# Performance work log

Measured on AMD Instinct MI355X. Metric: run time of the kernel, lower is better.

The kernel has to match this reference:

```python
import jax, jax.numpy as jnp
import numpy as np

D_MODEL = 2048
N_HEADS = 16
HEAD_DIM = D_MODEL // N_HEADS
SEGMENT_SIZE = 512
DILATION = 2
BATCH = 2
SEQ_LEN = 8192


def setup_inputs() -> dict:
    key = jax.random.key(0)
    k1, k2, k3 = jax.random.split(key, 3)
    x = jax.random.normal(k1, (BATCH, SEQ_LEN, D_MODEL), dtype=jnp.float32)
    Wqkv = jax.random.normal(k2, (3 * D_MODEL, D_MODEL), dtype=jnp.float32) * 0.02
    b_qkv = jnp.zeros((3 * D_MODEL,), dtype=jnp.float32)
    Wout = jax.random.normal(k3, (D_MODEL, D_MODEL), dtype=jnp.float32) * 0.02
    b_out = jnp.zeros((D_MODEL,), dtype=jnp.float32)
    return {"x": x, "Wqkv": Wqkv, "b_qkv": b_qkv, "Wout": Wout, "b_out": b_out}


def reference(x, Wqkv, b_qkv, Wout, b_out):
    B, S, D = x.shape
    H, hd = N_HEADS, HEAD_DIM
    # dilated segment gather: [B, n_seg, seg, D] strided by dilation -> [B, n_seg, L, D]
    xs = x.reshape(B, -1, SEGMENT_SIZE, D)[:, :, ::DILATION, :]
    N, L = xs.shape[1], xs.shape[2]
    # fused qkv projection (FlashMHA.Wqkv)
    qkv = jnp.einsum('bnld,ed->bnle', xs, Wqkv) + b_qkv  # [B,N,L,3D]
    q, k, v = jnp.split(qkv, 3, axis=-1)
    q = q.reshape(B, N, L, H, hd)
    k = k.reshape(B, N, L, H, hd)
    v = v.reshape(B, N, L, H, hd)
    scale = 1.0 / jnp.sqrt(jnp.asarray(hd, dtype=x.dtype))
    # per-segment attention over the dilated tokens
    scores = jnp.einsum('bnqhd,bnkhd->bnhqk', q, k) * scale  # [B,N,H,L,L]
    attn = jax.nn.softmax(scores, axis=-1)
    out = jnp.einsum('bnhqk,bnkhd->bnqhd', attn, v).reshape(B, N, L, D)
    # output projection (FlashMHA.out_proj)
    out = jnp.einsum('bnld,ed->bnle', out, Wout) + b_out
    # merge segments back: [B, N*L, D]
    return out.reshape(B, -1, D)
```

## Files before the change

kernel.cpp:

```cpp
#include <hip/hip_runtime.h>
#include <hip/hip_bf16.h>
#include <stdint.h>

#define DEVI __device__ __forceinline__

typedef __attribute__((ext_vector_type(8))) short bf16x8;
typedef __attribute__((ext_vector_type(4))) float f32x4;


DEVI unsigned short f2bf(float f) {
  unsigned int u = __float_as_uint(f);
  return (unsigned short)((u + 0x7fffu + ((u >> 16) & 1u)) >> 16);
}

DEVI void load_lds16(const void* g, void* l) {
  __builtin_amdgcn_global_load_lds(
      (const __attribute__((address_space(1))) unsigned int*)g,
      (__attribute__((address_space(3))) unsigned int*)l, 16, 0, 0);
}

DEVI bf16x8 ld8(const unsigned short* p) {
  return *reinterpret_cast<const bf16x8*>(p);
}

__global__ void k_prep(const float* __restrict__ x, unsigned short* __restrict__ xs,
                       const float* __restrict__ Wqkv, unsigned short* __restrict__ wq,
                       const float* __restrict__ Wout, unsigned short* __restrict__ wo) {
  const int bid = blockIdx.x;
  const float* src;
  unsigned short* dst;
  long i;
  if (bid < 16384) {
    int ii = bid * 256 + threadIdx.x;
    int r = ii >> 9;
    int c = (ii & 511) << 2;
    int b = r >> 12;
    int rem = r & 4095;
    int seg = rem >> 8;
    int lcl = rem & 255;
    long src_row = (long)b * 8192 + seg * 512 + lcl * 2;
    const float4 v = *reinterpret_cast<const float4*>(x + src_row * 2048 + c);
    uint2 o;
    o.x = f2bf(v.x) | ((unsigned)f2bf(v.y) << 16);
    o.y = f2bf(v.z) | ((unsigned)f2bf(v.w) << 16);
    *reinterpret_cast<uint2*>(xs + (long)r * 2048 + c) = o;
    return;
  } else if (bid < 28672) {
    i = (long)(bid - 16384) * 256 + threadIdx.x;
    src = Wqkv; dst = wq;
  } else {
    i = (long)(bid - 28672) * 256 + threadIdx.x;
    src = Wout; dst = wo;
  }
  const float4 v = *reinterpret_cast<const float4*>(src + i * 4);
  uint2 o;
  o.x = f2bf(v.x) | ((unsigned)f2bf(v.y) << 16);
  o.y = f2bf(v.z) | ((unsigned)f2bf(v.w) << 16);
  *reinterpret_cast<uint2*>(dst + i * 4) = o;
}


DEVI long stage_off(int s, int K) {
  int prow = s >> 3;
  int cs8 = s & 7;
  int c8 = cs8 ^ (prow & 7);
  int r = prow * 2 + (c8 >> 2);
  int k0 = (c8 & 3) << 3;
  return (long)r * K + k0;
}

#define FRAG_A(dst, mm)                                                      \
  { int r_ = wm * 128 + (mm) * 16 + lr;                                      \
    int p_ = r_ >> 1;                                                        \
    int cs_ = (((r_ & 1) << 2) | lq) ^ (p_ & 7);                             \
    dst = ld8(Ab_ + p_ * 64 + cs_ * 8); }
#define FRAG_B(dst, nn)                                                      \
  { int r_ = wn * 64 + (nn) * 16 + lr;                                       \
    int p_ = r_ >> 1;                                                        \
    int cs_ = (((r_ & 1) << 2) | lq) ^ (p_ & 7);                             \
    dst = ld8(Bb_ + p_ * 64 + cs_ * 8); }

#define STAGE_J(j)                                                           \
    load_lds16(pA0 + (j) * 32, (char*)smem + (((j) + 3) & 3) * 32768 + w * 1024);          \
    load_lds16(pA1 + (j) * 32, (char*)smem + (((j) + 3) & 3) * 32768 + 8192 + w * 1024);   \
    load_lds16(pB0 + (j) * 32, (char*)smem + (((j) + 3) & 3) * 32768 + 16384 + w * 1024);  \
    load_lds16(pB1 + (j) * 32, (char*)smem + (((j) + 3) & 3) * 32768 + 24576 + w * 1024);

#define HALF_J(j, DOSTAGE, VMLIT)                                            \
  {                                                                          \
    const unsigned short* Ab_ = smem + ((j) & 3) * 16384;                    \
    const unsigned short* Bb_ = Ab_ + 8192;                                  \
    if (DOSTAGE) { STAGE_J(j) }                                              \
    bf16x8 bfr[4], afr[8];                                                   \
    FRAG_B(bfr[0], 0) FRAG_B(bfr[1], 1) FRAG_B(bfr[2], 2) FRAG_B(bfr[3], 3)  \
    FRAG_A(afr[0], 0) FRAG_A(afr[1], 1) FRAG_A(afr[2], 2) FRAG_A(afr[3], 3)  \
    FRAG_A(afr[4], 4) FRAG_A(afr[5], 5) FRAG_A(afr[6], 6) FRAG_A(afr[7], 7)  \
    _Pragma("unroll")                                                        \
    for (int m_ = 0; m_ < 8; ++m_)                                           \
      _Pragma("unroll")                                                      \
      for (int n_ = 0; n_ < 4; ++n_)                                         \
        acc[m_][n_] = __builtin_amdgcn_mfma_f32_16x16x32_bf16(               \
            afr[m_], bfr[n_], acc[m_][n_], 0, 0, 0);                         \
    asm volatile("s_waitcnt vmcnt(" VMLIT ")" ::: "memory");                 \
    __builtin_amdgcn_s_barrier();                                            \
    asm volatile("" ::: "memory");                                           \
  }

template <bool BF16_OUT>
__global__ __launch_bounds__(512, 1)
void k_gemm(const unsigned short* __restrict__ A, const unsigned short* __restrict__ B,
            const float* __restrict__ bias, void* __restrict__ Cv, int N,
            int CHY, int CHX) {
  constexpr int K = 2048;
  __shared__ unsigned short smem[65536];
  const int nbx = N >> 8;
  const int xcd = blockIdx.x & 7;
  const int local = blockIdx.x >> 3;
  const int nchx = nbx / CHX;
  const int by = (xcd / nchx) * CHY + local / CHX;
  const int bx = (xcd % nchx) * CHX + local % CHX;
  const int t = threadIdx.x, w = t >> 6, l = t & 63;
  const int lr = l & 15, lq = l >> 4;
  const int wm = w >> 2, wn = w & 3;
  const unsigned short* Agb = A + (long)by * 256 * K;
  const unsigned short* Bgb = B + (long)bx * 256 * K;
  f32x4 acc[8][4] = {};

  const unsigned short* pA0 = Agb + stage_off(t, K);
  const unsigned short* pA1 = Agb + stage_off(512 + t, K);
  const unsigned short* pB0 = Bgb + stage_off(t, K);
  const unsigned short* pB1 = Bgb + stage_off(512 + t, K);

  load_lds16(pA0, (char*)smem + w * 1024);
  load_lds16(pA1, (char*)smem + 8192 + w * 1024);
  load_lds16(pB0, (char*)smem + 16384 + w * 1024);
  load_lds16(pB1, (char*)smem + 24576 + w * 1024);
  load_lds16(pA0 + 32, (char*)smem + 32768 + w * 1024);
  load_lds16(pA1 + 32, (char*)smem + 32768 + 8192 + w * 1024);
  load_lds16(pB0 + 32, (char*)smem + 32768 + 16384 + w * 1024);
  load_lds16(pB1 + 32, (char*)smem + 32768 + 24576 + w * 1024);
  load_lds16(pA0 + 64, (char*)smem + 65536 + w * 1024);
  load_lds16(pA1 + 64, (char*)smem + 65536 + 8192 + w * 1024);
  load_lds16(pB0 + 64, (char*)smem + 65536 + 16384 + w * 1024);
  load_lds16(pB1 + 64, (char*)smem + 65536 + 24576 + w * 1024);
  pA0 += 96; pA1 += 96; pB0 += 96; pB1 += 96;
  asm volatile("s_waitcnt vmcnt(8)" ::: "memory");
  __builtin_amdgcn_s_barrier();
  asm volatile("" ::: "memory");

  for (int hg = 0; hg < 15; ++hg) {
    HALF_J(0, true, "8") HALF_J(1, true, "8")
    HALF_J(2, true, "8") HALF_J(3, true, "8")
    pA0 += 128; pA1 += 128; pB0 += 128; pB1 += 128;
  }
  HALF_J(0, true, "8")
  HALF_J(1, false, "4")
  HALF_J(2, false, "0")
  HALF_J(3, false, "0")

  const long crow0 = (long)by * 256 + wm * 128;
  const int ccol0 = bx * 256 + wn * 64;
  float bv[4];
#pragma unroll
  for (int n = 0; n < 4; ++n) bv[n] = bias[ccol0 + n * 16 + lr];
  const int lrr = l >> 2;
  if (BF16_OUT) {
    unsigned short* Lw = smem + w * 1216;
    const int lcb = (l & 3) * 8;
#pragma unroll
    for (int m = 0; m < 8; ++m) {
#pragma unroll
      for (int n = 0; n < 4; ++n)
#pragma unroll
        for (int r = 0; r < 4; ++r)
          Lw[(lq * 4 + r) * 76 + n * 16 + lr] = f2bf(acc[m][n][r] + bv[n]);
      asm volatile("s_waitcnt lgkmcnt(0)" ::: "memory");
#pragma unroll
      for (int rd = 0; rd < 2; ++rd) {
        bf16x8 v = ld8(Lw + lrr * 76 + lcb + rd * 32);
        *reinterpret_cast<bf16x8*>((unsigned short*)Cv +
            (crow0 + m * 16 + lrr) * N + ccol0 + lcb + rd * 32) = v;
      }
    }
  } else {
    float* Lf = (float*)smem + w * 1216;
    const int lcf = (l & 3) * 4;
#pragma unroll
    for (int m = 0; m < 8; ++m) {
#pragma unroll
      for (int n = 0; n < 4; ++n)
#pragma unroll
        for (int r = 0; r < 4; ++r)
          Lf[(lq * 4 + r) * 76 + n * 16 + lr] = acc[m][n][r] + bv[n];
      asm volatile("s_waitcnt lgkmcnt(0)" ::: "memory");
#pragma unroll
      for (int rd = 0; rd < 4; ++rd) {
        float4 v = *reinterpret_cast<const float4*>(Lf + lrr * 76 + lcf + rd * 16);
        *reinterpret_cast<float4*>((float*)Cv +
            (crow0 + m * 16 + lrr) * N + ccol0 + lcf + rd * 16) = v;
      }
    }
  }
}

__global__ __launch_bounds__(512)
void k_attn(const unsigned short* __restrict__ qkv, unsigned short* __restrict__ aout) {
  __shared__ unsigned short smem[65536];
  unsigned short* Kl = smem;
  unsigned short* Vt = smem + 32768;
  const int p = blockIdx.x;
  const int h = p & 15;
  const long rb = (long)(p >> 4) * 256;
  const int t = threadIdx.x, w = t >> 6, l = t & 63;
  const int lr = l & 15, lq = l >> 4;

  const unsigned short* kb = qkv + rb * 6144 + 2048 + h * 128;
#pragma unroll
  for (int i = 0; i < 8; ++i) {
    int s = i * 512 + t;
    int row = s >> 4;
    int ch = (s & 15) ^ (row & 7);
    load_lds16(kb + (long)row * 6144 + ch * 8, (char*)Kl + i * 8192 + w * 1024);
  }
  const unsigned short* vb = qkv + rb * 6144 + 4096 + h * 128;
#pragma unroll
  for (int j0 = 0; j0 < 8; ++j0) {
    int k = j0 * 32 + (t >> 4);
    int d0 = (t & 15) * 8;
    bf16x8 v = ld8(vb + (long)k * 6144 + d0);
#pragma unroll
    for (int j = 0; j < 8; ++j) {
      int d = d0 + j;
      int ch = (k >> 3) ^ ((d ^ (d >> 3)) & 7);
      Vt[d * 256 + ch * 8 + (k & 7)] = (unsigned short)(short)v[j];
    }
  }
  const unsigned short* qb = qkv + (rb + w * 32) * 6144 + h * 128;
  bf16x8 qa[2][4];
#pragma unroll
  for (int m = 0; m < 2; ++m)
#pragma unroll
    for (int kt = 0; kt < 4; ++kt)
      qa[m][kt] = ld8(qb + (long)(m * 16 + lr) * 6144 + kt * 32 + lq * 8);

  __syncthreads();

  f32x4 sacc[2][16] = {};
  __builtin_amdgcn_s_setprio(1);
#pragma unroll
  for (int n = 0; n < 16; ++n) {
    int row = n * 16 + lr;
#pragma unroll
    for (int kt = 0; kt < 4; ++kt) {
      int ch = (kt * 4 + lq) ^ (row & 7);
      bf16x8 kf = ld8(Kl + row * 128 + ch * 8);
      sacc[0][n] = __builtin_amdgcn_mfma_f32_16x16x32_bf16(qa[0][kt], kf, sacc[0][n], 0, 0, 0);
      sacc[1][n] = __builtin_amdgcn_mfma_f32_16x16x32_bf16(qa[1][kt], kf, sacc[1][n], 0, 0, 0);
    }
  }
  __builtin_amdgcn_s_setprio(0);
  const float scale = 0.08838834764831845f;
  float mx[2][4], sm[2][4];
#pragma unroll
  for (int m = 0; m < 2; ++m)
#pragma unroll
    for (int r = 0; r < 4; ++r) {
      float v = sacc[m][0][r];
#pragma unroll
      for (int n = 1; n < 16; ++n) v = fmaxf(v, sacc[m][n][r]);
      mx[m][r] = v;
      sm[m][r] = 0.f;
    }
#pragma unroll
  for (int mk = 1; mk < 16; mk <<= 1)
#pragma unroll
    for (int m = 0; m < 2; ++m)
#pragma unroll
      for (int r = 0; r < 4; ++r)
        mx[m][r] = fmaxf(mx[m][r], __shfl_xor(mx[m][r], mk));
#pragma unroll
  for (int m = 0; m < 2; ++m)
#pragma unroll
    for (int n = 0; n < 16; ++n)
#pragma unroll
      for (int r = 0; r < 4; ++r) {
        float e = __expf((sacc[m][n][r] - mx[m][r]) * scale);
        sacc[m][n][r] = e;
        sm[m][r] += e;
      }
#pragma unroll
  for (int mk = 1; mk < 16; mk <<= 1)
#pragma unroll
    for (int m = 0; m < 2; ++m)
#pragma unroll
      for (int r = 0; r < 4; ++r)
        sm[m][r] += __shfl_xor(sm[m][r], mk);
  float ri[2][4];
#pragma unroll
  for (int m = 0; m < 2; ++m)
#pragma unroll
    for (int r = 0; r < 4; ++r) ri[m][r] = 1.0f / sm[m][r];

  unsigned int pb[2][16][2];
#pragma unroll
  for (int m = 0; m < 2; ++m)
#pragma unroll
    for (int n = 0; n < 16; ++n) {
      pb[m][n][0] = f2bf(sacc[m][n][0] * ri[m][0]) | ((unsigned)f2bf(sacc[m][n][1] * ri[m][1]) << 16);
      pb[m][n][1] = f2bf(sacc[m][n][2] * ri[m][2]) | ((unsigned)f2bf(sacc[m][n][3] * ri[m][3]) << 16);
    }

  __syncthreads();
  unsigned short* Pl = Kl + w * 4096;
  f32x4 oacc[2][8] = {};
#pragma unroll
  for (int half = 0; half < 2; ++half) {
#pragma unroll
    for (int m = 0; m < 2; ++m)
#pragma unroll
      for (int n = 0; n < 8; ++n) {
        int col = n * 16 + lr;
        int row0 = m * 16 + lq * 4;
#pragma unroll
        for (int pr = 0; pr < 2; ++pr) {
          unsigned int u = pb[m][half * 8 + n][pr];
          int ra = row0 + pr * 2, rbw = ra + 1;
          int ca = (col >> 3) ^ (ra & 7);
          int cb = (col >> 3) ^ (rbw & 7);
          Pl[ra * 128 + ca * 8 + (col & 7)] = (unsigned short)(u & 0xffffu);
          Pl[rbw * 128 + cb * 8 + (col & 7)] = (unsigned short)(u >> 16);
        }
      }
    __builtin_amdgcn_s_setprio(1);
#pragma unroll
    for (int kt = 0; kt < 4; ++kt) {
      bf16x8 pa[2];
#pragma unroll
      for (int m = 0; m < 2; ++m) {
        int row = m * 16 + lr;
        int ch = (kt * 4 + lq) ^ (row & 7);
        pa[m] = ld8(Pl + row * 128 + ch * 8);
      }
#pragma unroll
      for (int dt = 0; dt < 8; ++dt) {
        int d = dt * 16 + lr;
        int kg = half * 128 + kt * 32 + lq * 8;
        int ch = (kg >> 3) ^ ((d ^ (d >> 3)) & 7);
        bf16x8 vf = ld8(Vt + d * 256 + ch * 8);
        oacc[0][dt] = __builtin_amdgcn_mfma_f32_16x16x32_bf16(pa[0], vf, oacc[0][dt], 0, 0, 0);
        oacc[1][dt] = __builtin_amdgcn_mfma_f32_16x16x32_bf16(pa[1], vf, oacc[1][dt], 0, 0, 0);
      }
    }
    __builtin_amdgcn_s_setprio(0);
  }
  asm volatile("s_waitcnt lgkmcnt(0)" ::: "memory");
  unsigned short* Lo = Pl;
  unsigned short* ob = aout + (rb + w * 32) * 2048 + h * 128;
  const int orow = l >> 2;
  const int ocb = (l & 3) * 8;
#pragma unroll
  for (int m = 0; m < 2; ++m) {
#pragma unroll
    for (int dt = 0; dt < 8; ++dt)
#pragma unroll
      for (int r = 0; r < 4; ++r)
        Lo[(lq * 4 + r) * 136 + dt * 16 + lr] = f2bf(oacc[m][dt][r]);
    asm volatile("s_waitcnt lgkmcnt(0)" ::: "memory");
#pragma unroll
    for (int i = 0; i < 4; ++i) {
      bf16x8 v = ld8(Lo + orow * 136 + ocb + i * 32);
      *reinterpret_cast<bf16x8*>(ob + (long)(m * 16 + orow) * 2048 + ocb + i * 32) = v;
    }
    asm volatile("s_waitcnt lgkmcnt(0)" ::: "memory");
  }
}

extern "C" void kernel_launch(void* const* d_in, const int* in_sizes, int n_in,
                              void* d_out, int out_size, void* d_ws, size_t ws_size,
                              hipStream_t stream) {
  const float* x     = (const float*)d_in[0];
  const float* Wqkv  = (const float*)d_in[1];
  const float* b_qkv = (const float*)d_in[2];
  const float* Wout  = (const float*)d_in[3];
  const float* b_out = (const float*)d_in[4];
  float* out = (float*)d_out;

  char* ws = (char*)d_ws;
  unsigned short* xs   = (unsigned short*)(ws);
  unsigned short* aout = xs;
  unsigned short* wq   = (unsigned short*)(ws + 33554432);
  unsigned short* wo   = (unsigned short*)(ws + 58720256);
  unsigned short* qkv  = (unsigned short*)(ws + 67108864);

  k_prep<<<32768, 256, 0, stream>>>(x, xs, Wqkv, wq, Wout, wo);
  k_gemm<true><<<768, 512, 0, stream>>>(xs, wq, b_qkv, (void*)qkv, 6144, 16, 6);
  k_attn<<<512, 512, 0, stream>>>(qkv, aout);
  k_gemm<false><<<256, 512, 0, stream>>>(aout, wo, b_out, (void*)out, 2048, 8, 4);
}
```

Before: 323.5 us.

## Fuse dilated gather and bf16 conversion of x into QKV GEMM A-loading

Removes the separate pass that gathered every other row of x and wrote a bf16 copy. The QKV GEMM now reads fp32 x directly into registers, converts it to bf16 and writes it into LDS, software-pipelined two stages ahead, while B still uses direct global-to-LDS loads. This saves a full write and reread of the gathered activation. In exchange the GEMM reads twice the A bytes per tile (fp32) and spends extra VALU and register work on conversion, and every block re-reads the same fp32 rows of x across its 24 column tiles.

```diff
diff --git a/kernel.cpp b/kernel.cpp
--- a/kernel.cpp
+++ b/kernel.cpp
@@ -23,33 +23,29 @@
   return *reinterpret_cast<const bf16x8*>(p);
 }
 
-__global__ void k_prep(const float* __restrict__ x, unsigned short* __restrict__ xs,
-                       const float* __restrict__ Wqkv, unsigned short* __restrict__ wq,
+DEVI unsigned int pk2(float a, float b) {
+  __hip_bfloat162 h = __float22bfloat162_rn(float2{a, b});
+  return *reinterpret_cast<unsigned int*>(&h);
+}
+
+DEVI void write16(void* dst, const float4& x, const float4& y) {
+  uint4 u;
+  u.x = pk2(x.x, x.y); u.y = pk2(x.z, x.w);
+  u.z = pk2(y.x, y.y); u.w = pk2(y.z, y.w);
+  *reinterpret_cast<uint4*>(dst) = u;
+}
+
+__global__ void k_prep(const float* __restrict__ Wqkv, unsigned short* __restrict__ wq,
                        const float* __restrict__ Wout, unsigned short* __restrict__ wo) {
   const int bid = blockIdx.x;
   const float* src;
   unsigned short* dst;
   long i;
-  if (bid < 16384) {
-    int ii = bid * 256 + threadIdx.x;
-    int r = ii >> 9;
-    int c = (ii & 511) << 2;
-    int b = r >> 12;
-    int rem = r & 4095;
-    int seg = rem >> 8;
-    int lcl = rem & 255;
-    long src_row = (long)b * 8192 + seg * 512 + lcl * 2;
-    const float4 v = *reinterpret_cast<const float4*>(x + src_row * 2048 + c);
-    uint2 o;
-    o.x = f2bf(v.x) | ((unsigned)f2bf(v.y) << 16);
-    o.y = f2bf(v.z) | ((unsigned)f2bf(v.w) << 16);
-    *reinterpret_cast<uint2*>(xs + (long)r * 2048 + c) = o;
-    return;
-  } else if (bid < 28672) {
-    i = (long)(bid - 16384) * 256 + threadIdx.x;
+  if (bid < 12288) {
+    i = (long)bid * 256 + threadIdx.x;
     src = Wqkv; dst = wq;
   } else {
-    i = (long)(bid - 28672) * 256 + threadIdx.x;
+    i = (long)(bid - 12288) * 256 + threadIdx.x;
     src = Wout; dst = wo;
   }
   const float4 v = *reinterpret_cast<const float4*>(src + i * 4);
@@ -67,6 +63,14 @@
   int r = prow * 2 + (c8 >> 2);
   int k0 = (c8 & 3) << 3;
   return (long)r * K + k0;
+}
+
+DEVI long gath_off(int s) {
+  int prow = s >> 3;
+  int c8 = (s & 7) ^ (prow & 7);
+  int lrow = prow * 2 + (c8 >> 2);
+  int k0 = (c8 & 3) << 3;
+  return (long)(2 * lrow) * 2048 + k0;
 }
 
 #define FRAG_A(dst, mm)                                                      \
@@ -80,17 +84,7 @@
     int cs_ = (((r_ & 1) << 2) | lq) ^ (p_ & 7);                             \
     dst = ld8(Bb_ + p_ * 64 + cs_ * 8); }
 
-#define STAGE_J(j)                                                           \
-    load_lds16(pA0 + (j) * 32, (char*)smem + (((j) + 3) & 3) * 32768 + w * 1024);          \
-    load_lds16(pA1 + (j) * 32, (char*)smem + (((j) + 3) & 3) * 32768 + 8192 + w * 1024);   \
-    load_lds16(pB0 + (j) * 32, (char*)smem + (((j) + 3) & 3) * 32768 + 16384 + w * 1024);  \
-    load_lds16(pB1 + (j) * 32, (char*)smem + (((j) + 3) & 3) * 32768 + 24576 + w * 1024);
-
-#define HALF_J(j, DOSTAGE, VMLIT)                                            \
-  {                                                                          \
-    const unsigned short* Ab_ = smem + ((j) & 3) * 16384;                    \
-    const unsigned short* Bb_ = Ab_ + 8192;                                  \
-    if (DOSTAGE) { STAGE_J(j) }                                              \
+#define MFMA_BLOCK                                                           \
     bf16x8 bfr[4], afr[8];                                                   \
     FRAG_B(bfr[0], 0) FRAG_B(bfr[1], 1) FRAG_B(bfr[2], 2) FRAG_B(bfr[3], 3)  \
     FRAG_A(afr[0], 0) FRAG_A(afr[1], 1) FRAG_A(afr[2], 2) FRAG_A(afr[3], 3)  \
@@ -100,17 +94,153 @@
       _Pragma("unroll")                                                      \
       for (int n_ = 0; n_ < 4; ++n_)                                         \
         acc[m_][n_] = __builtin_amdgcn_mfma_f32_16x16x32_bf16(               \
-            afr[m_], bfr[n_], acc[m_][n_], 0, 0, 0);                         \
+            afr[m_], bfr[n_], acc[m_][n_], 0, 0, 0);
+
+#define GHALF(j, CONS, STG, VMLIT, PS)                                       \
+  {                                                                          \
+    if (CONS) {                                                              \
+      char* adst_ = (char*)smem + (((j) + 1) & 3) * 32768;                   \
+      write16(adst_ + t * 16, PS[0], PS[1]);                                 \
+      write16(adst_ + 8192 + t * 16, PS[2], PS[3]);                          \
+    }                                                                        \
+    if (STG) {                                                               \
+      PS[0] = *reinterpret_cast<const float4*>(pxA0 + (j) * 32);             \
+      PS[1] = *reinterpret_cast<const float4*>(pxA0 + (j) * 32 + 4);         \
+      PS[2] = *reinterpret_cast<const float4*>(pxA1 + (j) * 32);             \
+      PS[3] = *reinterpret_cast<const float4*>(pxA1 + (j) * 32 + 4);         \
+      load_lds16(pB0 + (j) * 32, (char*)smem + (((j) + 3) & 3) * 32768 + 16384 + w * 1024); \
+      load_lds16(pB1 + (j) * 32, (char*)smem + (((j) + 3) & 3) * 32768 + 24576 + w * 1024); \
+    }                                                                        \
+    const unsigned short* Ab_ = smem + ((j) & 3) * 16384;                    \
+    const unsigned short* Bb_ = Ab_ + 8192;                                  \
+    MFMA_BLOCK                                                               \
+    asm volatile("s_waitcnt vmcnt(" VMLIT ") lgkmcnt(0)" ::: "memory");      \
+    __builtin_amdgcn_s_barrier();                                            \
+    asm volatile("" ::: "memory");                                           \
+  }
+
+__global__ __launch_bounds__(512, 1)
+void k_gemm1g(const float* __restrict__ x, const unsigned short* __restrict__ B,
+              const float* __restrict__ bias, unsigned short* __restrict__ Cv,
+              int N, int CHY, int CHX) {
+  constexpr int K = 2048;
+  __shared__ unsigned short smem[65536];
+  const int nbx = N >> 8;
+  const int xcd = blockIdx.x & 7;
+  const int local = blockIdx.x >> 3;
+  const int nchx = nbx / CHX;
+  const int by = (xcd / nchx) * CHY + local / CHX;
+  const int bx = (xcd % nchx) * CHX + local % CHX;
+  const int t = threadIdx.x, w = t >> 6, l = t & 63;
+  const int lr = l & 15, lq = l >> 4;
+  const int wm = w >> 2, wn = w & 3;
+  const long brow = (long)(by >> 4) * 8192 + (long)(by & 15) * 512;
+  const float* xb = x + brow * 2048;
+  const unsigned short* Bgb = B + (long)bx * 256 * K;
+  f32x4 acc[8][4] = {};
+
+  const float* pxA0 = xb + gath_off(t);
+  const float* pxA1 = xb + gath_off(512 + t);
+  const unsigned short* pB0 = Bgb + stage_off(t, K);
+  const unsigned short* pB1 = Bgb + stage_off(512 + t, K);
+
+  float4 pE[4], pO[4];
+
+  {
+    float4 q0a = *reinterpret_cast<const float4*>(pxA0);
+    float4 q0b = *reinterpret_cast<const float4*>(pxA0 + 4);
+    float4 q0c = *reinterpret_cast<const float4*>(pxA1);
+    float4 q0d = *reinterpret_cast<const float4*>(pxA1 + 4);
+    load_lds16(pB0, (char*)smem + 16384 + w * 1024);
+    load_lds16(pB1, (char*)smem + 24576 + w * 1024);
+    float4 q1a = *reinterpret_cast<const float4*>(pxA0 + 32);
+    float4 q1b = *reinterpret_cast<const float4*>(pxA0 + 36);
+    float4 q1c = *reinterpret_cast<const float4*>(pxA1 + 32);
+    float4 q1d = *reinterpret_cast<const float4*>(pxA1 + 36);
+    load_lds16(pB0 + 32, (char*)smem + 32768 + 16384 + w * 1024);
+    load_lds16(pB1 + 32, (char*)smem + 32768 + 24576 + w * 1024);
+    float4 q2a = *reinterpret_cast<const float4*>(pxA0 + 64);
+    float4 q2b = *reinterpret_cast<const float4*>(pxA0 + 68);
+    float4 q2c = *reinterpret_cast<const float4*>(pxA1 + 64);
+    float4 q2d = *reinterpret_cast<const float4*>(pxA1 + 68);
+    load_lds16(pB0 + 64, (char*)smem + 65536 + 16384 + w * 1024);
+    load_lds16(pB1 + 64, (char*)smem + 65536 + 24576 + w * 1024);
+    write16((char*)smem + t * 16, q0a, q0b);
+    write16((char*)smem + 8192 + t * 16, q0c, q0d);
+    write16((char*)smem + 32768 + t * 16, q1a, q1b);
+    write16((char*)smem + 32768 + 8192 + t * 16, q1c, q1d);
+    write16((char*)smem + 65536 + t * 16, q2a, q2b);
+    write16((char*)smem + 65536 + 8192 + t * 16, q2c, q2d);
+  }
+  pxA0 += 96; pxA1 += 96; pB0 += 96; pB1 += 96;
+  asm volatile("s_waitcnt lgkmcnt(0)" ::: "memory");
+  __builtin_amdgcn_s_barrier();
+  asm volatile("" ::: "memory");
+
+  GHALF(0, false, true, "8",  pE)
+  GHALF(1, false, true, "12", pO)
+  GHALF(2, true,  true, "12", pE)
+  GHALF(3, true,  true, "12", pO)
+  pxA0 += 128; pxA1 += 128; pB0 += 128; pB1 += 128;
+  for (int hg = 1; hg < 15; ++hg) {
+    GHALF(0, true, true, "12", pE)
+    GHALF(1, true, true, "12", pO)
+    GHALF(2, true, true, "12", pE)
+    GHALF(3, true, true, "12", pO)
+    pxA0 += 128; pxA1 += 128; pB0 += 128; pB1 += 128;
+  }
+  GHALF(0, true,  true,  "12", pE)
+  GHALF(1, true,  false, "6",  pO)
+  GHALF(2, true,  false, "0",  pE)
+  GHALF(3, false, false, "0",  pO)
+
+  const long crow0 = (long)by * 256 + wm * 128;
+  const int ccol0 = bx * 256 + wn * 64;
+  float bv[4];
+#pragma unroll
+  for (int n = 0; n < 4; ++n) bv[n] = bias[ccol0 + n * 16 + lr];
+  const int lrr = l >> 2;
+  unsigned short* Lw = smem + w * 1216;
+  const int lcb = (l & 3) * 8;
+#pragma unroll
+  for (int m = 0; m < 8; ++m) {
+#pragma unroll
+    for (int n = 0; n < 4; ++n)
+#pragma unroll
+      for (int r = 0; r < 4; ++r)
+        Lw[(lq * 4 + r) * 76 + n * 16 + lr] = f2bf(acc[m][n][r] + bv[n]);
+    asm volatile("s_waitcnt lgkmcnt(0)" ::: "memory");
+#pragma unroll
+    for (int rd = 0; rd < 2; ++rd) {
+      bf16x8 v = ld8(Lw + lrr * 76 + lcb + rd * 32);
+      *reinterpret_cast<bf16x8*>(Cv +
+          (crow0 + m * 16 + lrr) * N + ccol0 + lcb + rd * 32) = v;
+    }
+    asm volatile("s_waitcnt lgkmcnt(0)" ::: "memory");
+  }
+}
+
+#define STAGE_J(j)                                                           \
+    load_lds16(pA0 + (j) * 32, (char*)smem + (((j) + 3) & 3) * 32768 + w * 1024);          \
+    load_lds16(pA1 + (j) * 32, (char*)smem + (((j) + 3) & 3) * 32768 + 8192 + w * 1024);   \
+    load_lds16(pB0 + (j) * 32, (char*)smem + (((j) + 3) & 3) * 32768 + 16384 + w * 1024);  \
+    load_lds16(pB1 + (j) * 32, (char*)smem + (((j) + 3) & 3) * 32768 + 24576 + w * 1024);
+
+#define HALF_J(j, DOSTAGE, VMLIT)                                            \
+  {                                                                          \
+    const unsigned short* Ab_ = smem + ((j) & 3) * 16384;                    \
+    const unsigned short* Bb_ = Ab_ + 8192;                                  \
+    if (DOSTAGE) { STAGE_J(j) }                                              \
+    MFMA_BLOCK                                                               \
     asm volatile("s_waitcnt vmcnt(" VMLIT ")" ::: "memory");                 \
     __builtin_amdgcn_s_barrier();                                            \
     asm volatile("" ::: "memory");                                           \
   }
 
-template <bool BF16_OUT>
 __global__ __launch_bounds__(512, 1)
-void k_gemm(const unsigned short* __restrict__ A, const unsigned short* __restrict__ B,
-            const float* __restrict__ bias, void* __restrict__ Cv, int N,
-            int CHY, int CHX) {
+void k_gemm2(const unsigned short* __restrict__ A, const unsigned short* __restrict__ B,
+             const float* __restrict__ bias, float* __restrict__ Cv, int N,
+             int CHY, int CHX) {
   constexpr int K = 2048;
   __shared__ unsigned short smem[65536];
   const int nbx = N >> 8;
@@ -164,42 +294,23 @@
 #pragma unroll
   for (int n = 0; n < 4; ++n) bv[n] = bias[ccol0 + n * 16 + lr];
   const int lrr = l >> 2;
-  if (BF16_OUT) {
-    unsigned short* Lw = smem + w * 1216;
-    const int lcb = (l & 3) * 8;
-#pragma unroll
-    for (int m = 0; m < 8; ++m) {
-#pragma unroll
-      for (int n = 0; n < 4; ++n)
-#pragma unroll
-        for (int r = 0; r < 4; ++r)
-          Lw[(lq * 4 + r) * 76 + n * 16 + lr] = f2bf(acc[m][n][r] + bv[n]);
-      asm volatile("s_waitcnt lgkmcnt(0)" ::: "memory");
-#pragma unroll
-      for (int rd = 0; rd < 2; ++rd) {
-        bf16x8 v = ld8(Lw + lrr * 76 + lcb + rd * 32);
-        *reinterpret_cast<bf16x8*>((unsigned short*)Cv +
-            (crow0 + m * 16 + lrr) * N + ccol0 + lcb + rd * 32) = v;
-      }
-    }
-  } else {
-    float* Lf = (float*)smem + w * 1216;
-    const int lcf = (l & 3) * 4;
-#pragma unroll
-    for (int m = 0; m < 8; ++m) {
-#pragma unroll
-      for (int n = 0; n < 4; ++n)
-#pragma unroll
-        for (int r = 0; r < 4; ++r)
-          Lf[(lq * 4 + r) * 76 + n * 16 + lr] = acc[m][n][r] + bv[n];
-      asm volatile("s_waitcnt lgkmcnt(0)" ::: "memory");
-#pragma unroll
-      for (int rd = 0; rd < 4; ++rd) {
-        float4 v = *reinterpret_cast<const float4*>(Lf + lrr * 76 + lcf + rd * 16);
-        *reinterpret_cast<float4*>((float*)Cv +
-            (crow0 + m * 16 + lrr) * N + ccol0 + lcf + rd * 16) = v;
-      }
-    }
+  float* Lf = (float*)smem + w * 1216;
+  const int lcf = (l & 3) * 4;
+#pragma unroll
+  for (int m = 0; m < 8; ++m) {
+#pragma unroll
+    for (int n = 0; n < 4; ++n)
+#pragma unroll
+      for (int r = 0; r < 4; ++r)
+        Lf[(lq * 4 + r) * 76 + n * 16 + lr] = acc[m][n][r] + bv[n];
+    asm volatile("s_waitcnt lgkmcnt(0)" ::: "memory");
+#pragma unroll
+    for (int rd = 0; rd < 4; ++rd) {
+      float4 v = *reinterpret_cast<const float4*>(Lf + lrr * 76 + lcf + rd * 16);
+      *reinterpret_cast<float4*>(Cv +
+          (crow0 + m * 16 + lrr) * N + ccol0 + lcf + rd * 16) = v;
+    }
+    asm volatile("s_waitcnt lgkmcnt(0)" ::: "memory");
   }
 }
 
@@ -386,14 +497,13 @@
   float* out = (float*)d_out;
 
   char* ws = (char*)d_ws;
-  unsigned short* xs   = (unsigned short*)(ws);
-  unsigned short* aout = xs;
+  unsigned short* aout = (unsigned short*)(ws);
   unsigned short* wq   = (unsigned short*)(ws + 33554432);
   unsigned short* wo   = (unsigned short*)(ws + 58720256);
   unsigned short* qkv  = (unsigned short*)(ws + 67108864);
 
-  k_prep<<<32768, 256, 0, stream>>>(x, xs, Wqkv, wq, Wout, wo);
-  k_gemm<true><<<768, 512, 0, stream>>>(xs, wq, b_qkv, (void*)qkv, 6144, 16, 6);
+  k_prep<<<16384, 256, 0, stream>>>(Wqkv, wq, Wout, wo);
+  k_gemm1g<<<768, 512, 0, stream>>>(x, wq, b_qkv, qkv, 6144, 16, 6);
   k_attn<<<512, 512, 0, stream>>>(qkv, aout);
-  k_gemm<false><<<256, 512, 0, stream>>>(aout, wo, b_out, (void*)out, 2048, 8, 4);
-}
+  k_gemm2<<<256, 512, 0, stream>>>(aout, wo, b_out, out, 2048, 8, 4);
+}
```

Measured after the change: 588.8 us. 1.82x slower.
